# Kernel optimization log

Measured on AMD Instinct MI355X. Metric: run time of the kernel, lower is better.

Reference implementation:

```python
import jax, jax.numpy as jnp
import numpy as np

V, H, B, T = 32000, 1024, 32, 256  # vocab, rnn_size, batch, seq_length


def setup_inputs() -> dict:
    key = jax.random.key(0)
    ks = jax.random.split(key, 6)
    s = 1.0 / np.sqrt(H)
    return {
        "input_data": jax.random.randint(ks[0], (B, T), 0, V, dtype=jnp.int32),
        "targets": jax.random.randint(ks[1], (B, T), 0, V, dtype=jnp.int32),
        "embedding": jax.random.uniform(ks[2], (V, H), minval=-1.0, maxval=1.0, dtype=jnp.float32),
        "softmax_b": jnp.zeros((V,), jnp.float32),
        "W0": (jax.random.normal(ks[3], (2 * H, 4 * H)) * s).astype(jnp.float32),
        "b0": jnp.zeros((4 * H,), jnp.float32),
        "W1": (jax.random.normal(ks[4], (2 * H, 4 * H)) * s).astype(jnp.float32),
        "b1": jnp.zeros((4 * H,), jnp.float32),
    }


def _lstm_step(x, c, h, W, b):
    # TF LSTMCell: gates i, j, f, o; forget_bias = 1.0
    z = jnp.concatenate([x, h], axis=-1) @ W + b  # [B, 4H]
    i, j, f, o = jnp.split(z, 4, axis=-1)
    c2 = c * jax.nn.sigmoid(f + 1.0) + jax.nn.sigmoid(i) * jnp.tanh(j)
    h2 = jax.nn.sigmoid(o) * jnp.tanh(c2)
    return c2, h2


def reference(input_data, targets, embedding, softmax_b, W0, b0, W1, b1):
    x = embedding[input_data]  # [B, T, H]
    Bb, Hh = x.shape[0], embedding.shape[1]
    zeros = jnp.zeros((Bb, Hh), x.dtype)
    init = ((zeros, zeros), (zeros, zeros))  # ((c0,h0),(c1,h1))

    def step(carry, xt):
        (c0, h0), (c1, h1) = carry
        c0, h0 = _lstm_step(xt, c0, h0, W0, b0)
        c1, h1 = _lstm_step(h0, c1, h1, W1, b1)
        return ((c0, h0), (c1, h1)), h1

    _, outs = jax.lax.scan(step, init, jnp.swapaxes(x, 0, 1))  # [T, B, H]
    output = jnp.swapaxes(outs, 0, 1).reshape(-1, Hh)  # [B*T, H]
    logits = output @ embedding.T + softmax_b  # tied softmax weights, [B*T, V]
    labels = targets.reshape(-1)
    logp = jax.nn.log_softmax(logits)
    loss = -jnp.take_along_axis(logp, labels[:, None], axis=1)[:, 0]
    cost = jnp.sum(loss) / Bb
    return logits, cost
```

## Files before the change

### kernel.cpp

```cpp
#include <hip/hip_runtime.h>
#include <hip/hip_bf16.h>

#define DEV static __device__ __forceinline__

typedef unsigned short u16;
typedef unsigned long long u64;
typedef __attribute__((ext_vector_type(8))) short short8;
typedef __attribute__((ext_vector_type(4))) float f32x4;

constexpr int V = 32000, H = 1024, B = 32, T = 256;
constexpr int BT = B * T;
constexpr int G  = 4 * H;
constexpr int NCH = V / 128;
constexpr int NWG2 = 256;
constexpr int RSTRIDE = 32 * 2048 + 2048;

constexpr size_t SZ_WT    = (size_t)G * 2048 * 2;
constexpr size_t OFF_W0T  = 0;
constexpr size_t OFF_W1T  = OFF_W0T + SZ_WT;
constexpr size_t OFF_EBF  = OFF_W1T + SZ_WT;
constexpr size_t OFF_XBF  = OFF_EBF + (size_t)V * H * 2;
constexpr size_t OFF_XP0  = OFF_XBF + (size_t)BT * H * 2;
constexpr size_t OFF_H1   = OFF_XP0 + (size_t)BT * G * 2;
constexpr size_t OFF_HSEQ = OFF_H1 + (size_t)BT * H * 2;
constexpr size_t SZ_HSEQ  = (size_t)(T + 2) * RSTRIDE * 2;
constexpr size_t OFF_SYNC = OFF_HSEQ + SZ_HSEQ;
constexpr size_t OFF_PMAX = OFF_SYNC + 8192;
constexpr size_t OFF_PSUM = OFF_PMAX + (size_t)BT * NCH * 4;
constexpr size_t OFF_LOSS = OFF_PSUM + (size_t)BT * NCH * 4;

DEV u16 f2bf(float x) {
  union { float f; unsigned int u; } v; v.f = x;
  unsigned int r = v.u + 0x7fffu + ((v.u >> 16) & 1u);
  return (u16)(r >> 16);
}
DEV float bf2f(u16 b) {
  union { unsigned int u; float f; } v; v.u = ((unsigned int)b) << 16;
  return v.f;
}
DEV float sigm(float x) { return 1.f / (1.f + expf(-x)); }

DEV void gload_lds16(const u16* g, u16* l) {
  __builtin_amdgcn_global_load_lds(
      (__attribute__((address_space(1))) void*)g,
      (__attribute__((address_space(3))) void*)l, 16, 0, 0);
}


__global__ void k_transpose_cvt(const float* __restrict__ in, u16* __restrict__ out,
                                int R, int C) {
  __shared__ float tile[32][33];
  int bc = blockIdx.x * 32, br = blockIdx.y * 32;
  int tx = threadIdx.x & 31, ty0 = threadIdx.x >> 5;
#pragma unroll
  for (int i = 0; i < 4; ++i) {
    int ty = ty0 + i * 8;
    tile[ty][tx] = in[(size_t)(br + ty) * C + bc + tx];
  }
  __syncthreads();
#pragma unroll
  for (int i = 0; i < 4; ++i) {
    int ty = ty0 + i * 8;
    out[(size_t)(bc + ty) * R + br + tx] = f2bf(tile[tx][ty]);
  }
}

__global__ void k_cvt_bf16(const float* __restrict__ in, u16* __restrict__ out, int n4) {
  int i = blockIdx.x * blockDim.x + threadIdx.x;
  int stride = gridDim.x * blockDim.x;
  for (; i < n4; i += stride) {
    float4 v = ((const float4*)in)[i];
    ushort4 o;
    o.x = f2bf(v.x); o.y = f2bf(v.y); o.z = f2bf(v.z); o.w = f2bf(v.w);
    ((ushort4*)out)[i] = o;
  }
}

__global__ void k_gather_x(const float* __restrict__ emb, const int* __restrict__ inp,
                           u16* __restrict__ Xbf) {
  int row = blockIdx.x;
  int t = row >> 5, b = row & 31;
  int tok = inp[b * T + t];
  const float4* src = (const float4*)(emb + (size_t)tok * H);
  ushort4* dst = (ushort4*)(Xbf + (size_t)row * H);
  float4 v = src[threadIdx.x];
  ushort4 o;
  o.x = f2bf(v.x); o.y = f2bf(v.y); o.z = f2bf(v.z); o.w = f2bf(v.w);
  dst[threadIdx.x] = o;
}

__global__ void k_zero(unsigned int* __restrict__ p, int nwords) {
  int i = blockIdx.x * blockDim.x + threadIdx.x;
  int stride = gridDim.x * blockDim.x;
  for (; i < nwords; i += stride) p[i] = 0u;
}

template <bool SM_EPI, int CMODE>
__global__ __launch_bounds__(256)
void k_gemm(const u16* __restrict__ A, int lda,
            const u16* __restrict__ Bt, int ldb,
            float* __restrict__ C, int ldc,
            const float* __restrict__ bias, int K,
            float* __restrict__ pmax, float* __restrict__ psum, int nch) {
  __shared__ alignas(16) u16 ldsA[128 * 32];
  __shared__ alignas(16) u16 ldsB[128 * 32];
  __shared__ float2 red[128][2];

  int tid = threadIdx.x, lane = tid & 63, w = tid >> 6;
  int row0 = blockIdx.y * 128, col0 = blockIdx.x * 128;
  int wr = w >> 1, wc = w & 1;
  int c15 = lane & 15, q4 = lane >> 4;

  const u16* ag[2]; const u16* bg[2];
#pragma unroll
  for (int j = 0; j < 2; ++j) {
    int r = (j * 4 + w) * 16 + (lane >> 2);
    int k = (lane & 3) * 8;
    ag[j] = A + (size_t)(row0 + r) * lda + k;
    bg[j] = Bt + (size_t)(col0 + r) * ldb + k;
  }
  u16* lA0 = ldsA + (size_t)(0 + w) * 512;
  u16* lA1 = ldsA + (size_t)(4 + w) * 512;
  u16* lB0 = ldsB + (size_t)(0 + w) * 512;
  u16* lB1 = ldsB + (size_t)(4 + w) * 512;

  f32x4 acc[4][4];
#pragma unroll
  for (int m = 0; m < 4; ++m)
#pragma unroll
    for (int n = 0; n < 4; ++n) acc[m][n] = (f32x4){0.f, 0.f, 0.f, 0.f};

  int nk = K >> 5;
  for (int kk = 0; kk < nk; ++kk) {
    int kb = kk * 32;
    gload_lds16(ag[0] + kb, lA0);
    gload_lds16(ag[1] + kb, lA1);
    gload_lds16(bg[0] + kb, lB0);
    gload_lds16(bg[1] + kb, lB1);
    __syncthreads();

    short8 af[4], bfr[4];
#pragma unroll
    for (int m = 0; m < 4; ++m)
      af[m] = *(const short8*)(ldsA + (wr * 64 + m * 16 + c15) * 32 + q4 * 8);
#pragma unroll
    for (int n = 0; n < 4; ++n)
      bfr[n] = *(const short8*)(ldsB + (wc * 64 + n * 16 + c15) * 32 + q4 * 8);
#pragma unroll
    for (int m = 0; m < 4; ++m)
#pragma unroll
      for (int n = 0; n < 4; ++n)
        acc[m][n] = __builtin_amdgcn_mfma_f32_16x16x32_bf16(af[m], bfr[n], acc[m][n], 0, 0, 0);
    __syncthreads();
  }

  float bias_n[4];
#pragma unroll
  for (int n = 0; n < 4; ++n) bias_n[n] = bias[col0 + wc * 64 + n * 16 + c15];

#pragma unroll
  for (int m = 0; m < 4; ++m) {
#pragma unroll
    for (int jr = 0; jr < 4; ++jr) {
      int r_g = row0 + wr * 64 + m * 16 + q4 * 4 + jr;
      float v[4];
#pragma unroll
      for (int n = 0; n < 4; ++n) {
        int c_g = col0 + wc * 64 + n * 16 + c15;
        float val = acc[m][n][jr] + bias_n[n];
        if (CMODE == 0) {
          C[(size_t)r_g * ldc + c_g] = val;
        } else {
          int tt = r_g >> 5, bb = r_g & 31;
          int q = c_g >> 10, wgup = (c_g & 1023) >> 3, uu = c_g & 7;
          ((u16*)C)[((((size_t)tt * 128 + wgup) * 32 + bb) * 32) + q * 8 + uu] = f2bf(val);
        }
        v[n] = val;
      }
      if (SM_EPI) {
        float mx = fmaxf(fmaxf(v[0], v[1]), fmaxf(v[2], v[3]));
        float s = __expf(v[0] - mx) + __expf(v[1] - mx) + __expf(v[2] - mx) + __expf(v[3] - mx);
#pragma unroll
        for (int d = 1; d < 16; d <<= 1) {
          float mo = __shfl_xor(mx, d, 64);
          float so = __shfl_xor(s, d, 64);
          float M2 = fmaxf(mx, mo);
          s = s * __expf(mx - M2) + so * __expf(mo - M2);
          mx = M2;
        }
        if (c15 == 0) red[wr * 64 + m * 16 + q4 * 4 + jr][wc] = make_float2(mx, s);
      }
    }
  }
  if (SM_EPI) {
    __syncthreads();
    if (tid < 128) {
      float2 a = red[tid][0], b2 = red[tid][1];
      float M2 = fmaxf(a.x, b2.x);
      float S = a.y * __expf(a.x - M2) + b2.y * __expf(b2.x - M2);
      pmax[(size_t)(row0 + tid) * nch + blockIdx.x] = M2;
      psum[(size_t)(row0 + tid) * nch + blockIdx.x] = S;
    }
  }
}


#define RED(w_, bt_, nt_, r_, c_) red[((((w_)*2 + (bt_)) * 2 + (nt_)) * 16 + (r_)) * 16 + (c_)]

DEV void grid_barrier(int* __restrict__ sync, int wg, int gen) {
  __syncthreads();
  if (threadIdx.x == 0) {
    int g = wg >> 4;
    int old = __hip_atomic_fetch_add(sync + g * 64, 1,
                                     __ATOMIC_RELAXED, __HIP_MEMORY_SCOPE_AGENT);
    if (old == 16 * gen - 1) {
      int m = __hip_atomic_fetch_add(sync + 16 * 64, 1,
                                     __ATOMIC_RELAXED, __HIP_MEMORY_SCOPE_AGENT);
      if (m == 16 * gen - 1)
        __hip_atomic_store(sync + 17 * 64, gen,
                           __ATOMIC_RELAXED, __HIP_MEMORY_SCOPE_AGENT);
    }
    while (__hip_atomic_load(sync + 17 * 64,
                             __ATOMIC_RELAXED, __HIP_MEMORY_SCOPE_AGENT) < gen)
      __builtin_amdgcn_s_sleep(2);
  }
  __builtin_amdgcn_sched_barrier(0);
  __syncthreads();
}

template <int KH, bool IS_L0>
DEV void lstm_role(const u16* __restrict__ WT,
                   const u16* __restrict__ xp0p,
                   const float* __restrict__ zb1,
                   u16* __restrict__ hseq, u16* __restrict__ H1bf,
                   int* __restrict__ sync, float* __restrict__ red,
                   int wgu, int wg) {
  constexpr int KOFF = IS_L0 ? 1024 : 0;
  constexpr int KS = KH / 4;
  constexpr int NKC = KS / 32;
  int tid = threadIdx.x, lane = tid & 63, w = tid >> 6;
  int c15 = lane & 15, q4 = lane >> 4;
  int eb = tid >> 3, eu = tid & 7;

  short8 wfr[2][NKC];
#pragma unroll
  for (int nt = 0; nt < 2; ++nt) {
    int lr = nt * 16 + c15;
    const u16* rp = WT + (size_t)((lr >> 3) * 1024 + wgu * 8 + (lr & 7)) * 2048
                    + KOFF + w * KS + q4 * 8;
#pragma unroll
    for (int kc = 0; kc < NKC; ++kc)
      wfr[nt][kc] = *(const short8*)(rp + kc * 32);
  }

  float zpc[4];
  if (!IS_L0) {
#pragma unroll
    for (int q = 0; q < 4; ++q) zpc[q] = zb1[q * 1024 + wgu * 8 + eu];
  }
  float creg = 0.f;

  for (int tick = 0; tick <= T; ++tick) {
    if (IS_L0 ? (tick < T) : (tick >= 1)) {
      float zp[4];
      if (IS_L0) {
#pragma unroll
        for (int q = 0; q < 4; ++q)
          zp[q] = bf2f(xp0p[((((size_t)tick * 128 + wgu) * 32 + eb) * 32) + q * 8 + eu]);
      } else {
#pragma unroll
        for (int q = 0; q < 4; ++q) zp[q] = zpc[q];
      }

      const u16* hread = hseq + (size_t)tick * RSTRIDE;
      f32x4 acc[2][2];
#pragma unroll
      for (int bt = 0; bt < 2; ++bt)
#pragma unroll
        for (int nt = 0; nt < 2; ++nt) acc[bt][nt] = (f32x4){0.f, 0.f, 0.f, 0.f};

#pragma unroll
      for (int kc = 0; kc < NKC; ++kc) {
        int kh = w * KS + kc * 32 + q4 * 8;
        short8 a0 = *(const short8*)(hread + (size_t)c15 * 2048 + kh);
        short8 a1 = *(const short8*)(hread + (size_t)(16 + c15) * 2048 + kh);
        acc[0][0] = __builtin_amdgcn_mfma_f32_16x16x32_bf16(a0, wfr[0][kc], acc[0][0], 0, 0, 0);
        acc[0][1] = __builtin_amdgcn_mfma_f32_16x16x32_bf16(a0, wfr[1][kc], acc[0][1], 0, 0, 0);
        acc[1][0] = __builtin_amdgcn_mfma_f32_16x16x32_bf16(a1, wfr[0][kc], acc[1][0], 0, 0, 0);
        acc[1][1] = __builtin_amdgcn_mfma_f32_16x16x32_bf16(a1, wfr[1][kc], acc[1][1], 0, 0, 0);
      }

#pragma unroll
      for (int bt = 0; bt < 2; ++bt)
#pragma unroll
        for (int nt = 0; nt < 2; ++nt)
#pragma unroll
          for (int jr = 0; jr < 4; ++jr)
            RED(w, bt, nt, q4 * 4 + jr, c15) = acc[bt][nt][jr];
      __syncthreads();

      int bt = eb >> 4, rr = eb & 15;
      float z[4];
#pragma unroll
      for (int q = 0; q < 4; ++q) {
        int lr = q * 8 + eu, nt = lr >> 4, cc = lr & 15;
        z[q] = RED(0, bt, nt, rr, cc) + RED(1, bt, nt, rr, cc) +
               RED(2, bt, nt, rr, cc) + RED(3, bt, nt, rr, cc) + zp[q];
      }
      float gi = sigm(z[0]);
      float gj = tanhf(z[1]);
      float gf = sigm(z[2] + 1.f);
      float go = sigm(z[3]);
      creg = creg * gf + gi * gj;
      float hv = go * tanhf(creg);

      int hb = (int)f2bf(hv);
      int hp = __shfl_xor(hb, 1, 64);
      if (!(tid & 1)) {
        unsigned int pack = (unsigned int)(u16)hb | ((unsigned int)(u16)hp << 16);
        u16* hwr = hseq + (size_t)(tick + 1) * RSTRIDE + (IS_L0 ? 0 : 1024);
        __hip_atomic_store((unsigned int*)(hwr + (size_t)eb * 2048 + wgu * 8 + eu), pack,
                           __ATOMIC_RELAXED, __HIP_MEMORY_SCOPE_AGENT);
        if (!IS_L0)
          *(unsigned int*)(H1bf + ((size_t)eb * T + (tick - 1)) * H + wgu * 8 + eu) = pack;
      }
    }
    grid_barrier(sync, wg, tick + 1);
  }
}

__global__ __launch_bounds__(256, 1)
void k_lstm_persistent(const u16* __restrict__ W0T, const u16* __restrict__ W1T,
                       const u16* __restrict__ xp0p, const float* __restrict__ b1,
                       u16* __restrict__ hseq, u16* __restrict__ H1bf,
                       int* __restrict__ sync) {
  __shared__ float red[4 * 2 * 2 * 16 * 16];
  int wg = blockIdx.x;
  if (wg < 128)
    lstm_role<1024, true>(W0T, xp0p, nullptr, hseq, H1bf, sync, red, wg, wg);
  else
    lstm_role<2048, false>(W1T, nullptr, b1, hseq, H1bf, sync, red, wg - 128, wg);
}

__global__ void k_rowfin(const float* __restrict__ pmax, const float* __restrict__ psum,
                         const float* __restrict__ Cl, const int* __restrict__ targets,
                         float* __restrict__ loss) {
  int row = blockIdx.x;
  int tid = threadIdx.x, lane = tid & 63, w = tid >> 6;
  float mx = -1e30f, s = 0.f;
  if (tid < NCH) { mx = pmax[(size_t)row * NCH + tid]; s = psum[(size_t)row * NCH + tid]; }
#pragma unroll
  for (int d = 1; d < 64; d <<= 1) {
    float mo = __shfl_xor(mx, d, 64);
    float so = __shfl_xor(s, d, 64);
    float M2 = fmaxf(mx, mo);
    s = s * __expf(mx - M2) + so * __expf(mo - M2);
    mx = M2;
  }
  __shared__ float2 wred[4];
  if (lane == 0) wred[w] = make_float2(mx, s);
  __syncthreads();
  if (tid == 0) {
    float M = wred[0].x, S = wred[0].y;
#pragma unroll
    for (int i = 1; i < 4; ++i) {
      float M2 = fmaxf(M, wred[i].x);
      S = S * __expf(M - M2) + wred[i].y * __expf(wred[i].x - M2);
      M = M2;
    }
    float logZ = M + logf(S);
    int tgt = targets[row];
    float xt = Cl[(size_t)row * V + tgt];
    loss[row] = logZ - xt;
  }
}

__global__ void k_cost(const float* __restrict__ loss, float* __restrict__ out) {
  int tid = threadIdx.x, lane = tid & 63, w = tid >> 6;
  float s = 0.f;
  for (int i = tid; i < BT; i += 256) s += loss[i];
#pragma unroll
  for (int d = 1; d < 64; d <<= 1) s += __shfl_xor(s, d, 64);
  __shared__ float ws4[4];
  if (lane == 0) ws4[w] = s;
  __syncthreads();
  if (tid == 0) out[0] = (ws4[0] + ws4[1] + ws4[2] + ws4[3]) * (1.0f / B);
}

extern "C" void kernel_launch(void* const* d_in, const int* in_sizes, int n_in,
                              void* d_out, int out_size, void* d_ws, size_t ws_size,
                              hipStream_t stream) {
  const int*   input_data = (const int*)d_in[0];
  const int*   targets    = (const int*)d_in[1];
  const float* emb        = (const float*)d_in[2];
  const float* softmax_b  = (const float*)d_in[3];
  const float* W0         = (const float*)d_in[4];
  const float* b0         = (const float*)d_in[5];
  const float* W1         = (const float*)d_in[6];
  const float* b1         = (const float*)d_in[7];
  float* out = (float*)d_out;
  char*  ws  = (char*)d_ws;

  u16*   W0T  = (u16*)(ws + OFF_W0T);
  u16*   W1T  = (u16*)(ws + OFF_W1T);
  u16*   Ebf  = (u16*)(ws + OFF_EBF);
  u16*   Xbf  = (u16*)(ws + OFF_XBF);
  u16*   xp0p = (u16*)(ws + OFF_XP0);
  u16*   H1bf = (u16*)(ws + OFF_H1);
  u16*   hseq = (u16*)(ws + OFF_HSEQ);
  int*   sync = (int*)(ws + OFF_SYNC);
  float* pmax = (float*)(ws + OFF_PMAX);
  float* psum = (float*)(ws + OFF_PSUM);
  float* lossb= (float*)(ws + OFF_LOSS);

  k_transpose_cvt<<<dim3(G / 32, 2048 / 32), 256, 0, stream>>>(W0, W0T, 2048, G);
  k_transpose_cvt<<<dim3(G / 32, 2048 / 32), 256, 0, stream>>>(W1, W1T, 2048, G);
  k_cvt_bf16<<<2048, 256, 0, stream>>>(emb, Ebf, V * H / 4);
  k_gather_x<<<BT, 256, 0, stream>>>(emb, input_data, Xbf);
  k_zero<<<64, 256, 0, stream>>>((unsigned int*)(ws + OFF_HSEQ), RSTRIDE);
  k_zero<<<1, 256, 0, stream>>>((unsigned int*)(ws + OFF_SYNC), 2048);

  k_gemm<false, 1><<<dim3(G / 128, BT / 128), 256, 0, stream>>>(
      Xbf, H, W0T, 2048, (float*)xp0p, G, b0, H, nullptr, nullptr, 0);

  k_lstm_persistent<<<dim3(NWG2), dim3(256), 0, stream>>>(
      W0T, W1T, xp0p, b1, hseq, H1bf, sync);

  k_gemm<true, 0><<<dim3(V / 128, BT / 128), 256, 0, stream>>>(
      H1bf, H, Ebf, H, out, V, softmax_b, H, pmax, psum, NCH);

  k_rowfin<<<BT, 256, 0, stream>>>(pmax, psum, out, targets, lossb);
  k_cost<<<1, 256, 0, stream>>>(lossb, out + (size_t)BT * V);
}
```

Baseline: 3.001 ms.

## Decouple LSTM layer barriers so layer 0 runs ahead, and swizzle GEMM tiles

Measured after the change: 3.190 ms. +6.3%, slower.

```diff
diff --git a/kernel.cpp b/kernel.cpp
--- a/kernel.cpp
+++ b/kernel.cpp
@@ -106,8 +106,13 @@
   __shared__ alignas(16) u16 ldsB[128 * 32];
   __shared__ float2 red[128][2];
 
+  unsigned nwg = gridDim.x * gridDim.y;
+  unsigned flat = blockIdx.y * gridDim.x + blockIdx.x;
+  unsigned nf = (flat & 7) * (nwg >> 3) + (flat >> 3);
+  unsigned bx = nf % gridDim.x, by = nf / gridDim.x;
+
   int tid = threadIdx.x, lane = tid & 63, w = tid >> 6;
-  int row0 = blockIdx.y * 128, col0 = blockIdx.x * 128;
+  int row0 = by * 128, col0 = bx * 128;
   int wr = w >> 1, wc = w & 1;
   int c15 = lane & 15, q4 = lane >> 4;
 
@@ -198,8 +203,8 @@
       float2 a = red[tid][0], b2 = red[tid][1];
       float M2 = fmaxf(a.x, b2.x);
       float S = a.y * __expf(a.x - M2) + b2.y * __expf(b2.x - M2);
-      pmax[(size_t)(row0 + tid) * nch + blockIdx.x] = M2;
-      psum[(size_t)(row0 + tid) * nch + blockIdx.x] = S;
+      pmax[(size_t)(row0 + tid) * nch + bx] = M2;
+      psum[(size_t)(row0 + tid) * nch + bx] = S;
     }
   }
 }
@@ -207,22 +212,21 @@
 
 #define RED(w_, bt_, nt_, r_, c_) red[((((w_)*2 + (bt_)) * 2 + (nt_)) * 16 + (r_)) * 16 + (c_)]
 
-DEV void grid_barrier(int* __restrict__ sync, int wg, int gen) {
+DEV void bar_sync(int* __restrict__ cnt, int target) {
   __syncthreads();
   if (threadIdx.x == 0) {
-    int g = wg >> 4;
-    int old = __hip_atomic_fetch_add(sync + g * 64, 1,
-                                     __ATOMIC_RELAXED, __HIP_MEMORY_SCOPE_AGENT);
-    if (old == 16 * gen - 1) {
-      int m = __hip_atomic_fetch_add(sync + 16 * 64, 1,
-                                     __ATOMIC_RELAXED, __HIP_MEMORY_SCOPE_AGENT);
-      if (m == 16 * gen - 1)
-        __hip_atomic_store(sync + 17 * 64, gen,
-                           __ATOMIC_RELAXED, __HIP_MEMORY_SCOPE_AGENT);
-    }
-    while (__hip_atomic_load(sync + 17 * 64,
-                             __ATOMIC_RELAXED, __HIP_MEMORY_SCOPE_AGENT) < gen)
-      __builtin_amdgcn_s_sleep(2);
+    __hip_atomic_fetch_add(cnt, 1, __ATOMIC_RELAXED, __HIP_MEMORY_SCOPE_AGENT);
+    while (__hip_atomic_load(cnt, __ATOMIC_RELAXED, __HIP_MEMORY_SCOPE_AGENT) < target)
+      __builtin_amdgcn_s_sleep(4);
+  }
+  __builtin_amdgcn_sched_barrier(0);
+  __syncthreads();
+}
+
+DEV void epoch_wait(const int* __restrict__ cnt, int target) {
+  if (threadIdx.x == 0) {
+    while (__hip_atomic_load(cnt, __ATOMIC_RELAXED, __HIP_MEMORY_SCOPE_AGENT) < target)
+      __builtin_amdgcn_s_sleep(4);
   }
   __builtin_amdgcn_sched_barrier(0);
   __syncthreads();
@@ -233,8 +237,8 @@
                    const u16* __restrict__ xp0p,
                    const float* __restrict__ zb1,
                    u16* __restrict__ hseq, u16* __restrict__ H1bf,
-                   int* __restrict__ sync, float* __restrict__ red,
-                   int wgu, int wg) {
+                   int* __restrict__ c_own, int* __restrict__ c_epoch,
+                   float* __restrict__ red, int wgu) {
   constexpr int KOFF = IS_L0 ? 1024 : 0;
   constexpr int KS = KH / 4;
   constexpr int NKC = KS / 32;
@@ -260,72 +264,75 @@
   }
   float creg = 0.f;
 
-  for (int tick = 0; tick <= T; ++tick) {
-    if (IS_L0 ? (tick < T) : (tick >= 1)) {
-      float zp[4];
-      if (IS_L0) {
-#pragma unroll
-        for (int q = 0; q < 4; ++q)
-          zp[q] = bf2f(xp0p[((((size_t)tick * 128 + wgu) * 32 + eb) * 32) + q * 8 + eu]);
-      } else {
-#pragma unroll
-        for (int q = 0; q < 4; ++q) zp[q] = zpc[q];
-      }
-
-      const u16* hread = hseq + (size_t)tick * RSTRIDE;
-      f32x4 acc[2][2];
-#pragma unroll
-      for (int bt = 0; bt < 2; ++bt)
-#pragma unroll
-        for (int nt = 0; nt < 2; ++nt) acc[bt][nt] = (f32x4){0.f, 0.f, 0.f, 0.f};
-
-#pragma unroll
-      for (int kc = 0; kc < NKC; ++kc) {
-        int kh = w * KS + kc * 32 + q4 * 8;
-        short8 a0 = *(const short8*)(hread + (size_t)c15 * 2048 + kh);
-        short8 a1 = *(const short8*)(hread + (size_t)(16 + c15) * 2048 + kh);
-        acc[0][0] = __builtin_amdgcn_mfma_f32_16x16x32_bf16(a0, wfr[0][kc], acc[0][0], 0, 0, 0);
-        acc[0][1] = __builtin_amdgcn_mfma_f32_16x16x32_bf16(a0, wfr[1][kc], acc[0][1], 0, 0, 0);
-        acc[1][0] = __builtin_amdgcn_mfma_f32_16x16x32_bf16(a1, wfr[0][kc], acc[1][0], 0, 0, 0);
-        acc[1][1] = __builtin_amdgcn_mfma_f32_16x16x32_bf16(a1, wfr[1][kc], acc[1][1], 0, 0, 0);
-      }
-
-#pragma unroll
-      for (int bt = 0; bt < 2; ++bt)
-#pragma unroll
-        for (int nt = 0; nt < 2; ++nt)
-#pragma unroll
-          for (int jr = 0; jr < 4; ++jr)
-            RED(w, bt, nt, q4 * 4 + jr, c15) = acc[bt][nt][jr];
-      __syncthreads();
-
-      int bt = eb >> 4, rr = eb & 15;
-      float z[4];
-#pragma unroll
-      for (int q = 0; q < 4; ++q) {
-        int lr = q * 8 + eu, nt = lr >> 4, cc = lr & 15;
-        z[q] = RED(0, bt, nt, rr, cc) + RED(1, bt, nt, rr, cc) +
-               RED(2, bt, nt, rr, cc) + RED(3, bt, nt, rr, cc) + zp[q];
-      }
-      float gi = sigm(z[0]);
-      float gj = tanhf(z[1]);
-      float gf = sigm(z[2] + 1.f);
-      float go = sigm(z[3]);
-      creg = creg * gf + gi * gj;
-      float hv = go * tanhf(creg);
-
-      int hb = (int)f2bf(hv);
-      int hp = __shfl_xor(hb, 1, 64);
-      if (!(tid & 1)) {
-        unsigned int pack = (unsigned int)(u16)hb | ((unsigned int)(u16)hp << 16);
-        u16* hwr = hseq + (size_t)(tick + 1) * RSTRIDE + (IS_L0 ? 0 : 1024);
-        __hip_atomic_store((unsigned int*)(hwr + (size_t)eb * 2048 + wgu * 8 + eu), pack,
-                           __ATOMIC_RELAXED, __HIP_MEMORY_SCOPE_AGENT);
-        if (!IS_L0)
-          *(unsigned int*)(H1bf + ((size_t)eb * T + (tick - 1)) * H + wgu * 8 + eu) = pack;
-      }
-    }
-    grid_barrier(sync, wg, tick + 1);
+  for (int it_t = 0; it_t < T; ++it_t) {
+    int t = IS_L0 ? it_t : it_t + 1;
+
+    if (!IS_L0) epoch_wait(c_epoch, 128 * t);
+
+    float zp[4];
+    if (IS_L0) {
+#pragma unroll
+      for (int q = 0; q < 4; ++q)
+        zp[q] = bf2f(xp0p[((((size_t)t * 128 + wgu) * 32 + eb) * 32) + q * 8 + eu]);
+    } else {
+#pragma unroll
+      for (int q = 0; q < 4; ++q) zp[q] = zpc[q];
+    }
+
+    const u16* hread = hseq + (size_t)t * RSTRIDE;
+    f32x4 acc[2][2];
+#pragma unroll
+    for (int bt = 0; bt < 2; ++bt)
+#pragma unroll
+      for (int nt = 0; nt < 2; ++nt) acc[bt][nt] = (f32x4){0.f, 0.f, 0.f, 0.f};
+
+#pragma unroll
+    for (int kc = 0; kc < NKC; ++kc) {
+      int kh = w * KS + kc * 32 + q4 * 8;
+      short8 a0 = *(const short8*)(hread + (size_t)c15 * 2048 + kh);
+      short8 a1 = *(const short8*)(hread + (size_t)(16 + c15) * 2048 + kh);
+      acc[0][0] = __builtin_amdgcn_mfma_f32_16x16x32_bf16(a0, wfr[0][kc], acc[0][0], 0, 0, 0);
+      acc[0][1] = __builtin_amdgcn_mfma_f32_16x16x32_bf16(a0, wfr[1][kc], acc[0][1], 0, 0, 0);
+      acc[1][0] = __builtin_amdgcn_mfma_f32_16x16x32_bf16(a1, wfr[0][kc], acc[1][0], 0, 0, 0);
+      acc[1][1] = __builtin_amdgcn_mfma_f32_16x16x32_bf16(a1, wfr[1][kc], acc[1][1], 0, 0, 0);
+    }
+
+#pragma unroll
+    for (int bt = 0; bt < 2; ++bt)
+#pragma unroll
+      for (int nt = 0; nt < 2; ++nt)
+#pragma unroll
+        for (int jr = 0; jr < 4; ++jr)
+          RED(w, bt, nt, q4 * 4 + jr, c15) = acc[bt][nt][jr];
+    __syncthreads();
+
+    int bt = eb >> 4, rr = eb & 15;
+    float z[4];
+#pragma unroll
+    for (int q = 0; q < 4; ++q) {
+      int lr = q * 8 + eu, nt = lr >> 4, cc = lr & 15;
+      z[q] = RED(0, bt, nt, rr, cc) + RED(1, bt, nt, rr, cc) +
+             RED(2, bt, nt, rr, cc) + RED(3, bt, nt, rr, cc) + zp[q];
+    }
+    float gi = sigm(z[0]);
+    float gj = tanhf(z[1]);
+    float gf = sigm(z[2] + 1.f);
+    float go = sigm(z[3]);
+    creg = creg * gf + gi * gj;
+    float hv = go * tanhf(creg);
+
+    int hb = (int)f2bf(hv);
+    int hp = __shfl_xor(hb, 1, 64);
+    if (!(tid & 1)) {
+      unsigned int pack = (unsigned int)(u16)hb | ((unsigned int)(u16)hp << 16);
+      u16* hwr = hseq + (size_t)(t + 1) * RSTRIDE + (IS_L0 ? 0 : 1024);
+      __hip_atomic_store((unsigned int*)(hwr + (size_t)eb * 2048 + wgu * 8 + eu), pack,
+                         __ATOMIC_RELAXED, __HIP_MEMORY_SCOPE_AGENT);
+      if (!IS_L0)
+        *(unsigned int*)(H1bf + ((size_t)eb * T + (t - 1)) * H + wgu * 8 + eu) = pack;
+    }
+
+    bar_sync(c_own, 128 * (IS_L0 ? t + 1 : t));
   }
 }
 
@@ -337,9 +344,9 @@
   __shared__ float red[4 * 2 * 2 * 16 * 16];
   int wg = blockIdx.x;
   if (wg < 128)
-    lstm_role<1024, true>(W0T, xp0p, nullptr, hseq, H1bf, sync, red, wg, wg);
+    lstm_role<1024, true>(W0T, xp0p, nullptr, hseq, H1bf, sync, nullptr, red, wg);
   else
-    lstm_role<2048, false>(W1T, nullptr, b1, hseq, H1bf, sync, red, wg - 128, wg);
+    lstm_role<2048, false>(W1T, nullptr, b1, hseq, H1bf, sync + 64, sync, red, wg - 128);
 }
 
 __global__ void k_rowfin(const float* __restrict__ pmax, const float* __restrict__ psum,
```
